# Optimization experiments

Measured on AMD Instinct MI355X. Metric: run time of the kernel, lower is better.

Reference implementation:

```python
import jax, jax.numpy as jnp
import numpy as np


def _pair_loss(s, r):
    # s: [N, 4] sampled lidar, r: [M, 4] raw lidar; use xyz only
    a = s[:, :3]
    b = r[:, :3]
    # pairwise Euclidean distances, [N, M] (torch.cdist p=2)
    sq = (jnp.sum(a * a, axis=1)[:, None]
          + jnp.sum(b * b, axis=1)[None, :]
          - 2.0 * (a @ b.T))
    dist = jnp.sqrt(jnp.maximum(sq, 0.0))
    # dist[argmin(dim=0), j] == min over rows; dist[i, argmin(dim=1)] == min over cols
    min_over_sampled = jnp.min(dist, axis=0)  # [M] nearest sampled point per raw point
    min_over_raw = jnp.min(dist, axis=1)      # [N] nearest raw point per sampled point
    LB = jnp.mean(min_over_sampled)
    LF = jnp.mean(min_over_raw)
    LM = jnp.max(min_over_raw)
    return 5.0 * LB + 1.0 * LF + LM


def setup_inputs() -> dict:
    key = jax.random.key(0)
    k1, k2 = jax.random.split(key)
    B, N, M = 2, 4096, 16384
    sampled = jax.random.normal(k1, (B, N, 4), dtype=jnp.float32)
    raw = jax.random.normal(k2, (B, M, 4), dtype=jnp.float32)
    return {"sampled": sampled, "raw": raw}


def reference(sampled, raw):
    # list of pairs == batch dim; loss averaged over pairs
    losses = jax.vmap(_pair_loss)(sampled, raw)  # [B]
    return jnp.mean(losses)
```

## Files before the change

kernel.cpp:

```cpp
#include <hip/hip_runtime.h>
#include <math.h>

constexpr int BB = 2, NN = 4096, MM = 16384;
constexpr int JS = 32;
constexpr int IG = 16;
constexpr int SC = 512;
constexpr int ST = SC / 16;
constexpr unsigned INFBITS = 0x7F800000u;
constexpr ushort ONEB = 0x3F80;

typedef __attribute__((ext_vector_type(8))) short  short8;
typedef __attribute__((ext_vector_type(8))) ushort ushort8;
typedef __attribute__((ext_vector_type(4))) float  f32x4;

__device__ __forceinline__ ushort f2bf(float f) {
    unsigned u = __float_as_uint(f);
    u += 0x7FFF + ((u >> 16) & 1);
    return (ushort)(u >> 16);
}
__device__ __forceinline__ void split2(float v, ushort& h, ushort& l) {
    h = f2bf(v);
    l = f2bf(v - __uint_as_float(((unsigned)h) << 16));
}

__global__ __launch_bounds__(256, 4) void pair_kernel(
    const float* __restrict__ sampled,
    const float* __restrict__ raw,
    float* __restrict__ rowpart,
    float* __restrict__ colpart)
{
    __shared__ ushort ldsB[ST * 512];
    __shared__ float  ldsCol[4][SC];

    const int js = blockIdx.x, ig = blockIdx.y, b = blockIdx.z;
    const int tid = threadIdx.x, w = tid >> 6, lane = tid & 63;
    const int p = lane & 15, c = lane >> 4;
    const int j0 = js * SC, i0 = ig * 256;

    const float4* rp4 = (const float4*)raw + (size_t)b * MM + j0;
    for (int t = tid; t < SC; t += 256) {
        float4 v = rp4[t];
        float n = fmaf(v.z, v.z, fmaf(v.y, v.y, v.x * v.x));
        ushort hx,lx,hy,ly,hz,lz,hn,ln;
        split2(v.x, hx, lx); split2(v.y, hy, ly);
        split2(v.z, hz, lz); split2(n, hn, ln);
        ushort* dst = ldsB + (t >> 4) * 512 + (t & 15) * 8;
        ushort8 zz = ushort8{0,0,0,0,0,0,0,0};
        *(ushort8*)(dst)       = ushort8{hx,hy,hz,lx,ly,lz,hx,hy};
        *(ushort8*)(dst + 128) = ushort8{hz,ONEB,ONEB,hn,ln,0,0,0};
        *(ushort8*)(dst + 256) = zz;
        *(ushort8*)(dst + 384) = zz;
    }

    short8 afr[4];
    const float4* sp4 = (const float4*)sampled + (size_t)b * NN + i0 + w * 64 + p;
#pragma unroll
    for (int f = 0; f < 4; ++f) {
        float4 v = sp4[f * 16];
        float n = fmaf(v.z, v.z, fmaf(v.y, v.y, v.x * v.x));
        ushort hx,lx,hy,ly,hz,lz,hn,ln;
        split2(-2.f * v.x, hx, lx); split2(-2.f * v.y, hy, ly);
        split2(-2.f * v.z, hz, lz); split2(n, hn, ln);
        ushort8 w0 = ushort8{hx,hy,hz,hx,hy,hz,lx,ly};
        ushort8 w1 = ushort8{lz,hn,ln,ONEB,ONEB,0,0,0};
        ushort8 zz = ushort8{0,0,0,0,0,0,0,0};
        ushort8 sel = (c == 0) ? w0 : ((c == 1) ? w1 : zz);
        afr[f] = *(short8*)&sel;
    }
    __syncthreads();

    const float INF = __uint_as_float(INFBITS);
    float racc[4][4];
#pragma unroll
    for (int f = 0; f < 4; ++f)
#pragma unroll
        for (int r = 0; r < 4; ++r) racc[f][r] = INF;

    const f32x4 zero = {0.f, 0.f, 0.f, 0.f};

    for (int jt = 0; jt < ST; ++jt) {
        short8 bf = *(const short8*)(ldsB + jt * 512 + lane * 8);
        f32x4 c0 = __builtin_amdgcn_mfma_f32_16x16x32_bf16(afr[0], bf, zero, 0, 0, 0);
        f32x4 c1 = __builtin_amdgcn_mfma_f32_16x16x32_bf16(afr[1], bf, zero, 0, 0, 0);
        f32x4 c2 = __builtin_amdgcn_mfma_f32_16x16x32_bf16(afr[2], bf, zero, 0, 0, 0);
        f32x4 c3 = __builtin_amdgcn_mfma_f32_16x16x32_bf16(afr[3], bf, zero, 0, 0, 0);
#pragma unroll
        for (int r = 0; r < 4; ++r) {
            racc[0][r] = fminf(racc[0][r], c0[r]);
            racc[1][r] = fminf(racc[1][r], c1[r]);
            racc[2][r] = fminf(racc[2][r], c2[r]);
            racc[3][r] = fminf(racc[3][r], c3[r]);
        }
        float m0 = fminf(fminf(c0[0], c0[1]), fminf(c0[2], c0[3]));
        float m1 = fminf(fminf(c1[0], c1[1]), fminf(c1[2], c1[3]));
        float m2 = fminf(fminf(c2[0], c2[1]), fminf(c2[2], c2[3]));
        float m3 = fminf(fminf(c3[0], c3[1]), fminf(c3[2], c3[3]));
        float m  = fminf(fminf(m0, m1), fminf(m2, m3));
        m = fminf(m, __shfl_xor(m, 16, 64));
        m = fminf(m, __shfl_xor(m, 32, 64));
        if (lane < 16) ldsCol[w][jt * 16 + lane] = m;
    }

#pragma unroll
    for (int mask = 1; mask < 16; mask <<= 1)
#pragma unroll
        for (int f = 0; f < 4; ++f)
#pragma unroll
            for (int r = 0; r < 4; ++r)
                racc[f][r] = fminf(racc[f][r], __shfl_xor(racc[f][r], mask, 64));
    if (p == 0) {
        float* rp = rowpart + ((size_t)js * BB + b) * NN + i0 + w * 64;
#pragma unroll
        for (int f = 0; f < 4; ++f)
#pragma unroll
            for (int r = 0; r < 4; ++r)
                rp[f * 16 + c * 4 + r] = fmaxf(racc[f][r], 0.f);
    }

    __syncthreads();
    float* cp = colpart + ((size_t)ig * BB + b) * MM + j0;
    for (int t = tid; t < SC; t += 256) {
        float v = fminf(fminf(ldsCol[0][t], ldsCol[1][t]),
                        fminf(ldsCol[2][t], ldsCol[3][t]));
        cp[t] = fmaxf(v, 0.f);
    }
}

__global__ __launch_bounds__(256) void reduce1_kernel(
    const float* __restrict__ rowpart,
    const float* __restrict__ colpart,
    float* __restrict__ part)
{
    const int k = blockIdx.x, b = k >> 6, s = k & 63;
    const int tid = threadIdx.x;
    const float INF = __uint_as_float(INFBITS);

    const int col = s * 256 + tid;
    float v = INF;
#pragma unroll 4
    for (int ig = 0; ig < IG; ++ig)
        v = fminf(v, colpart[((size_t)ig * BB + b) * MM + col]);
    float sB = sqrtf(v);

    const int row = s * 64 + (tid & 63);
    const int jq  = tid >> 6;
    float wv2 = INF;
#pragma unroll
    for (int q = 0; q < JS / 4; ++q)
        wv2 = fminf(wv2, rowpart[((size_t)(jq * (JS / 4) + q) * BB + b) * NN + row]);
    __shared__ float rred[4][64];
    rred[jq][tid & 63] = wv2;
    __syncthreads();
    float sF = 0.f, mF = 0.f;
    if (tid < 64) {
        float rmn = fminf(fminf(rred[0][tid], rred[1][tid]),
                          fminf(rred[2][tid], rred[3][tid]));
        float d = sqrtf(rmn);
        sF = d; mF = d;
    }

    for (int m = 1; m < 64; m <<= 1) {
        sB += __shfl_xor(sB, m, 64);
        sF += __shfl_xor(sF, m, 64);
        mF = fmaxf(mF, __shfl_xor(mF, m, 64));
    }
    __shared__ float red[3][4];
    const int lane = tid & 63, wvi = tid >> 6;
    if (lane == 0) { red[0][wvi] = sB; red[1][wvi] = sF; red[2][wvi] = mF; }
    __syncthreads();
    if (tid == 0) {
        part[k * 3 + 0] = red[0][0] + red[0][1] + red[0][2] + red[0][3];
        part[k * 3 + 1] = red[1][0] + red[1][1] + red[1][2] + red[1][3];
        part[k * 3 + 2] = fmaxf(fmaxf(red[2][0], red[2][1]),
                                fmaxf(red[2][2], red[2][3]));
    }
}

__global__ void reduce2_kernel(const float* __restrict__ part,
                               float* __restrict__ out)
{
    const int tid = threadIdx.x;
    float sB = part[tid * 3 + 0];
    float sF = part[tid * 3 + 1];
    float mF = part[tid * 3 + 2];
    for (int m = 1; m < 64; m <<= 1) {
        sB += __shfl_xor(sB, m, 64);
        sF += __shfl_xor(sF, m, 64);
        mF = fmaxf(mF, __shfl_xor(mF, m, 64));
    }
    __shared__ float red[2][3];
    if ((tid & 63) == 0) { red[tid >> 6][0] = sB; red[tid >> 6][1] = sF; red[tid >> 6][2] = mF; }
    __syncthreads();
    if (tid == 0) {
        float l0 = 5.f * red[0][0] / (float)MM + red[0][1] / (float)NN + red[0][2];
        float l1 = 5.f * red[1][0] / (float)MM + red[1][1] / (float)NN + red[1][2];
        *out = 0.5f * (l0 + l1);
    }
}

extern "C" void kernel_launch(void* const* d_in, const int* in_sizes, int n_in,
                              void* d_out, int out_size, void* d_ws, size_t ws_size,
                              hipStream_t stream) {
    const float* sampled = (const float*)d_in[0];
    const float* raw     = (const float*)d_in[1];
    float* rowpart = (float*)d_ws;
    float* colpart = rowpart + (size_t)JS * BB * NN;
    float* part    = colpart + (size_t)IG * BB * MM;
    float* out     = (float*)d_out;

    pair_kernel<<<dim3(JS, IG, BB), 256, 0, stream>>>(sampled, raw, rowpart, colpart);
    reduce1_kernel<<<128, 256, 0, stream>>>(rowpart, colpart, part);
    reduce2_kernel<<<1, 128, 0, stream>>>(part, out);
}
```

Before: 37.29 us.

## Switch to 32x32x16 MFMA tiles and fuse final reduction via last-block counter

Replaces the 16x16x32 bf16 MFMA, which padded half of K with zeros, with a 32x32x16 MFMA whose K of 16 exactly fits the split-bf16 distance encoding. This halves the MFMA count and the padded LDS data per tile. The cross-lane shuffle reductions and the row-index mapping are rewritten to match the new accumulator layout. The separate final reduction kernel is folded into reduce_kernel using an atomic counter and a last-block pattern, saving one launch. The counter is reset by one thread inside pair_kernel.

```diff
diff --git a/kernel.cpp b/kernel.cpp
--- a/kernel.cpp
+++ b/kernel.cpp
@@ -5,13 +5,13 @@
 constexpr int JS = 32;
 constexpr int IG = 16;
 constexpr int SC = 512;
-constexpr int ST = SC / 16;
+constexpr int ST = SC / 32;
 constexpr unsigned INFBITS = 0x7F800000u;
 constexpr ushort ONEB = 0x3F80;
 
-typedef __attribute__((ext_vector_type(8))) short  short8;
-typedef __attribute__((ext_vector_type(8))) ushort ushort8;
-typedef __attribute__((ext_vector_type(4))) float  f32x4;
+typedef __attribute__((ext_vector_type(8)))  short  short8;
+typedef __attribute__((ext_vector_type(8)))  ushort ushort8;
+typedef __attribute__((ext_vector_type(16))) float  f32x16;
 
 __device__ __forceinline__ ushort f2bf(float f) {
     unsigned u = __float_as_uint(f);
@@ -22,20 +22,29 @@
     h = f2bf(v);
     l = f2bf(v - __uint_as_float(((unsigned)h) << 16));
 }
+__device__ __forceinline__ float vmin16(const f32x16& c) {
+    float a0 = fminf(fminf(c[0], c[1]),  fminf(c[2], c[3]));
+    float a1 = fminf(fminf(c[4], c[5]),  fminf(c[6], c[7]));
+    float a2 = fminf(fminf(c[8], c[9]),  fminf(c[10], c[11]));
+    float a3 = fminf(fminf(c[12], c[13]), fminf(c[14], c[15]));
+    return fminf(fminf(a0, a1), fminf(a2, a3));
+}
 
 __global__ __launch_bounds__(256, 4) void pair_kernel(
     const float* __restrict__ sampled,
     const float* __restrict__ raw,
     float* __restrict__ rowpart,
-    float* __restrict__ colpart)
+    float* __restrict__ colpart,
+    unsigned* __restrict__ counter)
 {
     __shared__ ushort ldsB[ST * 512];
     __shared__ float  ldsCol[4][SC];
 
     const int js = blockIdx.x, ig = blockIdx.y, b = blockIdx.z;
     const int tid = threadIdx.x, w = tid >> 6, lane = tid & 63;
-    const int p = lane & 15, c = lane >> 4;
     const int j0 = js * SC, i0 = ig * 256;
+
+    if (js == 0 && ig == 0 && b == 0 && tid == 0) *counter = 0u;
 
     const float4* rp4 = (const float4*)raw + (size_t)b * MM + j0;
     for (int t = tid; t < SC; t += 256) {
@@ -44,77 +53,67 @@
         ushort hx,lx,hy,ly,hz,lz,hn,ln;
         split2(v.x, hx, lx); split2(v.y, hy, ly);
         split2(v.z, hz, lz); split2(n, hn, ln);
-        ushort* dst = ldsB + (t >> 4) * 512 + (t & 15) * 8;
-        ushort8 zz = ushort8{0,0,0,0,0,0,0,0};
+        ushort* dst = ldsB + (t >> 5) * 512 + (t & 31) * 8;
         *(ushort8*)(dst)       = ushort8{hx,hy,hz,lx,ly,lz,hx,hy};
-        *(ushort8*)(dst + 128) = ushort8{hz,ONEB,ONEB,hn,ln,0,0,0};
-        *(ushort8*)(dst + 256) = zz;
-        *(ushort8*)(dst + 384) = zz;
-    }
-
-    short8 afr[4];
-    const float4* sp4 = (const float4*)sampled + (size_t)b * NN + i0 + w * 64 + p;
-#pragma unroll
-    for (int f = 0; f < 4; ++f) {
-        float4 v = sp4[f * 16];
+        *(ushort8*)(dst + 256) = ushort8{hz,ONEB,ONEB,hn,ln,0,0,0};
+    }
+
+    short8 afr[2];
+    const float4* sp4 = (const float4*)sampled + (size_t)b * NN + i0 + w * 64 + (lane & 31);
+    const int half = lane >> 5;
+#pragma unroll
+    for (int f = 0; f < 2; ++f) {
+        float4 v = sp4[f * 32];
         float n = fmaf(v.z, v.z, fmaf(v.y, v.y, v.x * v.x));
         ushort hx,lx,hy,ly,hz,lz,hn,ln;
         split2(-2.f * v.x, hx, lx); split2(-2.f * v.y, hy, ly);
         split2(-2.f * v.z, hz, lz); split2(n, hn, ln);
         ushort8 w0 = ushort8{hx,hy,hz,hx,hy,hz,lx,ly};
         ushort8 w1 = ushort8{lz,hn,ln,ONEB,ONEB,0,0,0};
-        ushort8 zz = ushort8{0,0,0,0,0,0,0,0};
-        ushort8 sel = (c == 0) ? w0 : ((c == 1) ? w1 : zz);
+        ushort8 sel = half ? w1 : w0;
         afr[f] = *(short8*)&sel;
     }
     __syncthreads();
 
     const float INF = __uint_as_float(INFBITS);
-    float racc[4][4];
-#pragma unroll
-    for (int f = 0; f < 4; ++f)
-#pragma unroll
-        for (int r = 0; r < 4; ++r) racc[f][r] = INF;
-
-    const f32x4 zero = {0.f, 0.f, 0.f, 0.f};
-
+    float racc0[16], racc1[16];
+#pragma unroll
+    for (int r = 0; r < 16; ++r) { racc0[r] = INF; racc1[r] = INF; }
+
+    const f32x16 zero = {0.f,0.f,0.f,0.f,0.f,0.f,0.f,0.f,
+                         0.f,0.f,0.f,0.f,0.f,0.f,0.f,0.f};
+
+#pragma unroll 1
     for (int jt = 0; jt < ST; ++jt) {
         short8 bf = *(const short8*)(ldsB + jt * 512 + lane * 8);
-        f32x4 c0 = __builtin_amdgcn_mfma_f32_16x16x32_bf16(afr[0], bf, zero, 0, 0, 0);
-        f32x4 c1 = __builtin_amdgcn_mfma_f32_16x16x32_bf16(afr[1], bf, zero, 0, 0, 0);
-        f32x4 c2 = __builtin_amdgcn_mfma_f32_16x16x32_bf16(afr[2], bf, zero, 0, 0, 0);
-        f32x4 c3 = __builtin_amdgcn_mfma_f32_16x16x32_bf16(afr[3], bf, zero, 0, 0, 0);
-#pragma unroll
-        for (int r = 0; r < 4; ++r) {
-            racc[0][r] = fminf(racc[0][r], c0[r]);
-            racc[1][r] = fminf(racc[1][r], c1[r]);
-            racc[2][r] = fminf(racc[2][r], c2[r]);
-            racc[3][r] = fminf(racc[3][r], c3[r]);
+        f32x16 c0 = __builtin_amdgcn_mfma_f32_32x32x16_bf16(afr[0], bf, zero, 0, 0, 0);
+        f32x16 c1 = __builtin_amdgcn_mfma_f32_32x32x16_bf16(afr[1], bf, zero, 0, 0, 0);
+#pragma unroll
+        for (int r = 0; r < 16; ++r) {
+            racc0[r] = fminf(racc0[r], c0[r]);
+            racc1[r] = fminf(racc1[r], c1[r]);
         }
-        float m0 = fminf(fminf(c0[0], c0[1]), fminf(c0[2], c0[3]));
-        float m1 = fminf(fminf(c1[0], c1[1]), fminf(c1[2], c1[3]));
-        float m2 = fminf(fminf(c2[0], c2[1]), fminf(c2[2], c2[3]));
-        float m3 = fminf(fminf(c3[0], c3[1]), fminf(c3[2], c3[3]));
-        float m  = fminf(fminf(m0, m1), fminf(m2, m3));
-        m = fminf(m, __shfl_xor(m, 16, 64));
+        float m = fminf(vmin16(c0), vmin16(c1));
         m = fminf(m, __shfl_xor(m, 32, 64));
-        if (lane < 16) ldsCol[w][jt * 16 + lane] = m;
-    }
-
-#pragma unroll
-    for (int mask = 1; mask < 16; mask <<= 1)
-#pragma unroll
-        for (int f = 0; f < 4; ++f)
-#pragma unroll
-            for (int r = 0; r < 4; ++r)
-                racc[f][r] = fminf(racc[f][r], __shfl_xor(racc[f][r], mask, 64));
-    if (p == 0) {
+        if (lane < 32) ldsCol[w][jt * 32 + lane] = m;
+    }
+
+#pragma unroll
+    for (int mask = 1; mask < 32; mask <<= 1) {
+#pragma unroll
+        for (int r = 0; r < 16; ++r) {
+            racc0[r] = fminf(racc0[r], __shfl_xor(racc0[r], mask, 64));
+            racc1[r] = fminf(racc1[r], __shfl_xor(racc1[r], mask, 64));
+        }
+    }
+    if ((lane & 31) == 0) {
         float* rp = rowpart + ((size_t)js * BB + b) * NN + i0 + w * 64;
 #pragma unroll
-        for (int f = 0; f < 4; ++f)
-#pragma unroll
-            for (int r = 0; r < 4; ++r)
-                rp[f * 16 + c * 4 + r] = fmaxf(racc[f][r], 0.f);
+        for (int r = 0; r < 16; ++r) {
+            const int row = (r & 3) + 8 * (r >> 2) + 4 * half;
+            rp[row]      = fmaxf(racc0[r], 0.f);
+            rp[32 + row] = fmaxf(racc1[r], 0.f);
+        }
     }
 
     __syncthreads();
@@ -126,10 +125,12 @@
     }
 }
 
-__global__ __launch_bounds__(256) void reduce1_kernel(
+__global__ __launch_bounds__(256) void reduce_kernel(
     const float* __restrict__ rowpart,
     const float* __restrict__ colpart,
-    float* __restrict__ part)
+    float* __restrict__ part,
+    unsigned* __restrict__ counter,
+    float* __restrict__ out)
 {
     const int k = blockIdx.x, b = k >> 6, s = k & 63;
     const int tid = threadIdx.x;
@@ -168,32 +169,38 @@
     const int lane = tid & 63, wvi = tid >> 6;
     if (lane == 0) { red[0][wvi] = sB; red[1][wvi] = sF; red[2][wvi] = mF; }
     __syncthreads();
+
+    __shared__ bool isLast;
     if (tid == 0) {
         part[k * 3 + 0] = red[0][0] + red[0][1] + red[0][2] + red[0][3];
         part[k * 3 + 1] = red[1][0] + red[1][1] + red[1][2] + red[1][3];
         part[k * 3 + 2] = fmaxf(fmaxf(red[2][0], red[2][1]),
                                 fmaxf(red[2][2], red[2][3]));
-    }
-}
-
-__global__ void reduce2_kernel(const float* __restrict__ part,
-                               float* __restrict__ out)
-{
-    const int tid = threadIdx.x;
-    float sB = part[tid * 3 + 0];
-    float sF = part[tid * 3 + 1];
-    float mF = part[tid * 3 + 2];
+        __threadfence();
+        isLast = (atomicAdd(counter, 1u) == 127u);
+    }
+    __syncthreads();
+    if (!isLast) return;
+
+    __threadfence();
+    volatile const float* vp = part;
+    float fB = 0.f, fF = 0.f, fM = 0.f;
+    if (tid < 128) {
+        fB = vp[tid * 3 + 0]; fF = vp[tid * 3 + 1]; fM = vp[tid * 3 + 2];
+    }
     for (int m = 1; m < 64; m <<= 1) {
-        sB += __shfl_xor(sB, m, 64);
-        sF += __shfl_xor(sF, m, 64);
-        mF = fmaxf(mF, __shfl_xor(mF, m, 64));
-    }
-    __shared__ float red[2][3];
-    if ((tid & 63) == 0) { red[tid >> 6][0] = sB; red[tid >> 6][1] = sF; red[tid >> 6][2] = mF; }
+        fB += __shfl_xor(fB, m, 64);
+        fF += __shfl_xor(fF, m, 64);
+        fM = fmaxf(fM, __shfl_xor(fM, m, 64));
+    }
+    __shared__ float fin[2][3];
+    if (tid < 128 && (tid & 63) == 0) {
+        fin[tid >> 6][0] = fB; fin[tid >> 6][1] = fF; fin[tid >> 6][2] = fM;
+    }
     __syncthreads();
     if (tid == 0) {
-        float l0 = 5.f * red[0][0] / (float)MM + red[0][1] / (float)NN + red[0][2];
-        float l1 = 5.f * red[1][0] / (float)MM + red[1][1] / (float)NN + red[1][2];
+        float l0 = 5.f * fin[0][0] / (float)MM + fin[0][1] / (float)NN + fin[0][2];
+        float l1 = 5.f * fin[1][0] / (float)MM + fin[1][1] / (float)NN + fin[1][2];
         *out = 0.5f * (l0 + l1);
     }
 }
@@ -206,9 +213,9 @@
     float* rowpart = (float*)d_ws;
     float* colpart = rowpart + (size_t)JS * BB * NN;
     float* part    = colpart + (size_t)IG * BB * MM;
+    unsigned* counter = (unsigned*)(part + 3 * 128);
     float* out     = (float*)d_out;
 
-    pair_kernel<<<dim3(JS, IG, BB), 256, 0, stream>>>(sampled, raw, rowpart, colpart);
-    reduce1_kernel<<<128, 256, 0, stream>>>(rowpart, colpart, part);
-    reduce2_kernel<<<1, 128, 0, stream>>>(part, out);
-}
+    pair_kernel<<<dim3(JS, IG, BB), 256, 0, stream>>>(sampled, raw, rowpart, colpart, counter);
+    reduce_kernel<<<128, 256, 0, stream>>>(rowpart, colpart, part, counter, out);
+}
```

Result: slower. 38.35 us (+2.8%).
